# Optimization experiments

Measured on AMD Instinct MI355X. Metric: run time of the kernel, lower is better.

The kernel has to match this reference:

```python
import jax, jax.numpy as jnp
import numpy as np

B, T, V, D, E = 128, 50, 10000, 512, 2048


def setup_inputs() -> dict:
    key = jax.random.key(0)
    ks = jax.random.split(key, 14)
    s = 1.0 / np.sqrt(D)
    enc_out = jax.random.normal(ks[0], (B, E), jnp.float32)
    captions = jax.random.randint(ks[1], (B, T), 0, V)
    caplens = jax.random.randint(ks[2], (B, 1), 2, T + 1)
    caplens = caplens.at[0, 0].set(T)  # ensure max(caplens)-1 == T-1 (static shape)
    return {
        "enc_out": enc_out,
        "captions": captions,
        "caplens": caplens,
        "emb_W": jax.random.normal(ks[3], (V, D), jnp.float32),
        "W_ih": jax.random.uniform(ks[4], (4 * D, D), jnp.float32, -s, s),
        "W_hh": jax.random.uniform(ks[5], (4 * D, D), jnp.float32, -s, s),
        "b_ih": jax.random.uniform(ks[6], (4 * D,), jnp.float32, -s, s),
        "b_hh": jax.random.uniform(ks[7], (4 * D,), jnp.float32, -s, s),
        "fc_W": jax.random.uniform(ks[8], (V, D), jnp.float32, -s, s),
        "fc_b": jnp.zeros((V,), jnp.float32),
        "init_h_W": jax.random.uniform(ks[9], (D, E), jnp.float32, -s, s),
        "init_h_b": jnp.zeros((D,), jnp.float32),
        "init_c_W": jax.random.uniform(ks[10], (D, E), jnp.float32, -s, s),
        "init_c_b": jnp.zeros((D,), jnp.float32),
    }


def reference(enc_out, captions, caplens, emb_W, W_ih, W_hh, b_ih, b_hh,
              fc_W, fc_b, init_h_W, init_h_b, init_c_W, init_c_b):
    # Sort by caption length, descending (manual packing in the torch code).
    cl = caplens[:, 0]
    sort_idx = jnp.argsort(-cl)
    cl = cl[sort_idx]
    enc = enc_out[sort_idx]
    caps = captions[sort_idx]

    # init_states
    h0 = enc @ init_h_W.T + init_h_b  # [B, D]
    c0 = enc @ init_c_W.T + init_c_b

    emb = emb_W[caps]                  # [B, T, D] embedding gather
    dec_lens = cl - 1                  # decode lengths, max == T-1 by construction
    Tm = caps.shape[1] - 1             # static max timesteps

    # active-row mask per timestep: row b is active at step t iff t < dec_lens[b]
    masks = jnp.arange(Tm)[:, None] < dec_lens[None, :]   # [Tm, B]
    xs = jnp.moveaxis(emb[:, :Tm, :], 1, 0)               # [Tm, B, D]

    def step(carry, inp):
        h, c = carry
        x_t, m = inp                                      # [B,D], [B]
        gates = x_t @ W_ih.T + b_ih + h @ W_hh.T + b_hh   # [B, 4D]
        i, f, g, o = jnp.split(gates, 4, axis=-1)
        i = jax.nn.sigmoid(i)
        f = jax.nn.sigmoid(f)
        g = jnp.tanh(g)
        o = jax.nn.sigmoid(o)
        c_new = f * c + i * g
        h_new = o * jnp.tanh(c_new)
        mm = m[:, None]
        # inactive (shorter) rows keep their old state; torch never touches them
        h = jnp.where(mm, h_new, h)
        c = jnp.where(mm, c_new, c)
        # dropout in eval mode == identity; preds only written for active rows
        preds = jnp.where(mm, h_new @ fc_W.T + fc_b, 0.0)  # [B, V]
        return (h, c), preds

    (_, _), preds = jax.lax.scan(step, (h0, c0), (xs, masks))  # [Tm, B, V]
    predictions = jnp.moveaxis(preds, 0, 1)                    # [B, Tm, V]
    return predictions, caps, dec_lens, sort_idx
```

## Files before the change

### kernel.cpp

```cpp
#include <hip/hip_runtime.h>
#include <hip/hip_bf16.h>
#include <math.h>

typedef __attribute__((ext_vector_type(8))) short short8;
typedef __attribute__((ext_vector_type(4))) float f32x4;
typedef __attribute__((ext_vector_type(4))) unsigned short us4;
typedef unsigned short u16;
typedef unsigned long long u64;

#define TM 49
#define NV 10000
#define NLSTM 64
#define NFC 192
#define SMEM_BYTES 133184

__device__ __forceinline__ u16 f2bf(float f) {
    union { float f; unsigned u; } v; v.f = f;
    unsigned r = v.u + 0x7fffu + ((v.u >> 16) & 1u);
    return (u16)(r >> 16);
}
__device__ __forceinline__ float fsigm(float x) {
    return 1.0f / (1.0f + __expf(-x));
}
__device__ __forceinline__ float ftanh(float x) {
    float x2 = fminf(fmaxf(x + x, -30.0f), 30.0f);
    float e = __expf(x2);
    return (e - 1.0f) / (e + 1.0f);
}

__device__ __forceinline__ short8 ld_cp128(const u16* p) {
    short8 r;
    asm volatile("global_load_dwordx4 %0, %1, off sc0 sc1" : "=v"(r) : "v"(p));
    return r;
}
__device__ __forceinline__ void st_cp16(u16* p, unsigned v) {
    asm volatile("global_store_short %0, %1, off sc0 sc1" :: "v"(p), "v"(v) : "memory");
}
__device__ __forceinline__ void st_cp32f(float* p, float v) {
    asm volatile("global_store_dword %0, %1, off sc0 sc1" :: "v"(p), "v"(v) : "memory");
}
__device__ __forceinline__ void st_cp32u(unsigned* p, unsigned v) {
    asm volatile("global_store_dword %0, %1, off sc0 sc1" :: "v"(p), "v"(v) : "memory");
}
__device__ __forceinline__ unsigned ld_cp32_wait(const unsigned* p) {
    unsigned r;
    asm volatile("global_load_dword %0, %1, off sc0 sc1\n\ts_waitcnt vmcnt(0)"
                 : "=v"(r) : "v"(p) : "memory");
    return r;
}

__global__ __launch_bounds__(128) void k_sort(
    const int* __restrict__ caplens, const int* __restrict__ captions,
    const float* __restrict__ bih, const float* __restrict__ bhh,
    int* __restrict__ sidx, int* __restrict__ decl, int* __restrict__ capsS,
    float* __restrict__ bsum, float* __restrict__ out_tail,
    unsigned* __restrict__ flags, unsigned* __restrict__ xcnt,
    int* __restrict__ offs, int* __restrict__ rowmap, int* __restrict__ maskmap)
{
    __shared__ int s_cl[128];
    __shared__ int s_si[128];
    __shared__ int s_dl[128];
    __shared__ int s_n[49];
    __shared__ int s_off[50];
    __shared__ int s_moff[128];
    int tid = threadIdx.x;
    for (int k = tid; k < 2048; k += 128)
        __hip_atomic_store(&flags[k], 0u, __ATOMIC_RELAXED, __HIP_MEMORY_SCOPE_AGENT);
    for (int k = tid; k < 1568; k += 128)
        __hip_atomic_store(&xcnt[k], 0u, __ATOMIC_RELAXED, __HIP_MEMORY_SCOPE_AGENT);
    int my = caplens[tid];
    s_cl[tid] = my;
    __syncthreads();
    int r = 0;
    for (int j = 0; j < 128; j++) {
        int cj = s_cl[j];
        if (cj > my || (cj == my && j < tid)) r++;
    }
    s_si[r] = tid;
    __syncthreads();
    int src = s_si[tid];
    sidx[tid] = src;
    int dl = s_cl[src] - 1;
    decl[tid] = dl;
    s_dl[tid] = dl;
    out_tail[6400 + tid] = (float)dl;
    out_tail[6528 + tid] = (float)src;
    for (int t = 0; t < 50; t++) {
        int tok = captions[src * 50 + t];
        capsS[tid * 50 + t] = tok;
        out_tail[tid * 50 + t] = (float)tok;
    }
    for (int k = tid; k < 2048; k += 128) bsum[k] = bih[k] + bhh[k];
    __syncthreads();
    if (tid < 49) {
        int c = 0;
        for (int b = 0; b < 128; b++) c += (s_dl[b] > tid);
        s_n[tid] = c;
    }
    __syncthreads();
    if (tid == 0) {
        int a = 0;
        for (int t = 0; t < 49; t++) { s_off[t] = a; a += s_n[t]; }
        s_off[49] = a;
        int m = 0;
        for (int b = 0; b < 128; b++) { s_moff[b] = m; m += 49 - s_dl[b]; }
    }
    __syncthreads();
    if (tid < 50) offs[tid] = s_off[tid];
    for (int t = 0; t < dl; t++) rowmap[s_off[t] + tid] = t * 128 + tid;
    int mo = s_moff[tid];
    for (int t = dl; t < 49; t++) maskmap[mo + (t - dl)] = tid * 49 + t;
}

__global__ __launch_bounds__(256) void k_cvt(
    const float* __restrict__ Wih, const float* __restrict__ Whh,
    const float* __restrict__ fcW, const float* __restrict__ ihW,
    const float* __restrict__ icW,
    u16* __restrict__ WihB, u16* __restrict__ WhhB,
    u16* __restrict__ fcWB, u16* __restrict__ WhcB)
{
    int idx = blockIdx.x * 256 + threadIdx.x;
    const float* src; u16* dst; int o;
    if (idx < 262144)        { src = Wih; dst = WihB; o = idx; }
    else if (idx < 524288)   { src = Whh; dst = WhhB; o = idx - 262144; }
    else if (idx < 1804288)  { src = fcW; dst = fcWB; o = idx - 524288; }
    else if (idx < 2066432)  { src = ihW; dst = WhcB; o = idx - 1804288; }
    else                     { src = icW; dst = WhcB + 1048576; o = idx - 2066432; }
    f32x4 v = *(const f32x4*)&src[(size_t)o * 4];
    us4 b = { f2bf(v.x), f2bf(v.y), f2bf(v.z), f2bf(v.w) };
    *(us4*)&dst[(size_t)o * 4] = b;
}

__global__ __launch_bounds__(256) void k_gather(
    const float* __restrict__ enc, const float* __restrict__ embW,
    const int* __restrict__ sidx, const int* __restrict__ capsS,
    u16* __restrict__ encB, u16* __restrict__ Xemb)
{
    int idx = blockIdx.x * 256 + threadIdx.x;
    if (idx < 65536) {
        int b = idx >> 9, k4 = idx & 511;
        f32x4 v = *(const f32x4*)&enc[(size_t)sidx[b] * 2048 + k4 * 4];
        us4 o = { f2bf(v.x), f2bf(v.y), f2bf(v.z), f2bf(v.w) };
        *(us4*)&encB[(size_t)b * 2048 + k4 * 4] = o;
    } else {
        int j = idx - 65536;
        int row = j >> 7, k4 = j & 127;
        int t = row >> 7, b = row & 127;
        int tok = capsS[b * 50 + t];
        f32x4 v = *(const f32x4*)&embW[(size_t)tok * 512 + k4 * 4];
        us4 o = { f2bf(v.x), f2bf(v.y), f2bf(v.z), f2bf(v.w) };
        *(us4*)&Xemb[(size_t)row * 512 + k4 * 4] = o;
    }
}

__device__ __forceinline__ void tile_gemm_plain(
    const u16* __restrict__ A, int lda, const u16* __restrict__ B, int ldb,
    int K, int tid, u16 (*As)[40], u16 (*Bs)[40], f32x4 acc[4][4])
{
    const int w = tid >> 6, l = tid & 63;
    const int wr = (w >> 1) * 64, wc = (w & 1) * 64;
    const int lr = l & 15, lg = l >> 4;
    for (int k0 = 0; k0 < K; k0 += 32) {
        __syncthreads();
        #pragma unroll
        for (int i = 0; i < 2; i++) {
            int L = tid * 8 + i * 2048;
            int r = L >> 5, c = L & 31;
            *(short8*)&As[r][c] = *(const short8*)&A[(size_t)r * lda + k0 + c];
            *(short8*)&Bs[r][c] = *(const short8*)&B[(size_t)r * ldb + k0 + c];
        }
        __syncthreads();
        short8 af[4], bfr[4];
        #pragma unroll
        for (int m = 0; m < 4; m++) af[m] = *(const short8*)&As[wr + m * 16 + lr][lg * 8];
        #pragma unroll
        for (int n = 0; n < 4; n++) bfr[n] = *(const short8*)&Bs[wc + n * 16 + lr][lg * 8];
        #pragma unroll
        for (int m = 0; m < 4; m++)
            #pragma unroll
            for (int n = 0; n < 4; n++)
                acc[m][n] = __builtin_amdgcn_mfma_f32_16x16x32_bf16(af[m], bfr[n], acc[m][n], 0, 0, 0);
    }
}

__global__ __launch_bounds__(256, 1) void lstm_fc(
    const u16* __restrict__ Whh, float* __restrict__ X,
    u16* __restrict__ hb0, u16* __restrict__ hb1,
    u16* __restrict__ HnewC,
    const int* __restrict__ decl, unsigned* __restrict__ flags,
    unsigned* __restrict__ xcnt,
    const int* __restrict__ offs, const int* __restrict__ rowmap,
    const int* __restrict__ maskmap,
    const u16* __restrict__ fcWB, const float* __restrict__ fcb,
    const u16* __restrict__ encB, const u16* __restrict__ WhcB,
    const u16* __restrict__ WihB, const u16* __restrict__ Xemb,
    const float* __restrict__ bsum,
    const float* __restrict__ ihb, const float* __restrict__ icb,
    float* __restrict__ out)
{
    extern __shared__ char smem[];
    const int tid = threadIdx.x;
    const int wg = blockIdx.x;

    if (wg < NLSTM) {
        u16 (*As)[520] = (u16(*)[520])smem;
        u16 (*Bsi)[520] = (u16(*)[520])(smem + 33280);
        const int rb = wg >> 4, cb = wg & 15;
        const int w = tid >> 6, l = tid & 63;
        const int hi = w >> 1, lo = w & 1;
        const int lr = l & 15, lg = l >> 4;
        unsigned* myflag = &flags[(rb * 16 + cb) * 32];

        const int col = cb * 32 + lo * 16 + lr;
        int rowg[4];
        #pragma unroll
        for (int i = 0; i < 4; i++) rowg[i] = rb * 32 + hi * 16 + lg * 4 + i;

        f32x4 acch = {}, accc = {};
        for (int kq = 0; kq < 4; kq++) {
            __syncthreads();
            #pragma unroll
            for (int i = 0; i < 8; i++) {
                int L = tid * 8 + i * 2048;
                int r = L >> 9, cc = L & 511;
                *(short8*)&As[r][cc] =
                    *(const short8*)&encB[(size_t)(rb * 32 + r) * 2048 + kq * 512 + cc];
                *(short8*)&Bsi[r][cc] =
                    *(const short8*)&WhcB[(size_t)(cb * 32 + r) * 2048 + kq * 512 + cc];
            }
            __syncthreads();
            #pragma unroll
            for (int kk = 0; kk < 16; kk++) {
                short8 a = *(const short8*)&As[hi * 16 + lr][kk * 32 + lg * 8];
                short8 b = *(const short8*)&Bsi[lo * 16 + lr][kk * 32 + lg * 8];
                acch = __builtin_amdgcn_mfma_f32_16x16x32_bf16(a, b, acch, 0, 0, 0);
            }
            __syncthreads();
            #pragma unroll
            for (int i = 0; i < 8; i++) {
                int L = tid * 8 + i * 2048;
                int r = L >> 9, cc = L & 511;
                *(short8*)&Bsi[r][cc] =
                    *(const short8*)&WhcB[(size_t)(512 + cb * 32 + r) * 2048 + kq * 512 + cc];
            }
            __syncthreads();
            #pragma unroll
            for (int kk = 0; kk < 16; kk++) {
                short8 a = *(const short8*)&As[hi * 16 + lr][kk * 32 + lg * 8];
                short8 b = *(const short8*)&Bsi[lo * 16 + lr][kk * 32 + lg * 8];
                accc = __builtin_amdgcn_mfma_f32_16x16x32_bf16(a, b, accc, 0, 0, 0);
            }
        }

        int edec[4];
        f32x4 creg;
        us4 hreg;
        #pragma unroll
        for (int i = 0; i < 4; i++) {
            edec[i] = decl[rowg[i]];
            creg[i] = accc[i] + icb[col];
            hreg[i] = f2bf(acch[i] + ihb[col]);
            st_cp16(&hb0[(size_t)rowg[i] * 512 + col], (unsigned)hreg[i]);
        }
        asm volatile("s_waitcnt vmcnt(0)" ::: "memory");
        __syncthreads();
        if (tid == 0) st_cp32u(myflag, 1u);

        short8 bq[4][16];
        #pragma unroll
        for (int q = 0; q < 4; q++) {
            const u16* base = &Whh[(size_t)(q * 512 + cb * 32 + lo * 16 + lr) * 512 + lg * 8];
            #pragma unroll
            for (int kk = 0; kk < 16; kk++)
                bq[q][kk] = *(const short8*)&base[kk * 32];
        }
        #pragma unroll
        for (int q = 0; q < 4; q++)
            #pragma unroll
            for (int kk = 0; kk < 16; kk++)
                asm volatile("" : "+v"(bq[q][kk]));

        for (int t = 0; t < TM; t++) {
            const u16* hin = (t & 1) ? hb1 : hb0;
            u16* hout = (t & 1) ? hb0 : hb1;

            if (tid < 64) {
                unsigned tgt_h = (unsigned)(t + 1);
                while (true) {
                    bool ok = true;
                    if (tid < 16)
                        ok = (ld_cp32_wait(&flags[(rb * 16 + tid) * 32]) >= tgt_h);
                    else if (tid == 16)
                        ok = (ld_cp32_wait(&xcnt[t * 32]) >= 16u);
                    if (__all(ok)) break;
                }
            }
            __syncthreads();

            float xq[4][4];
            #pragma unroll
            for (int q = 0; q < 4; q++)
                #pragma unroll
                for (int i = 0; i < 4; i++)
                    xq[q][i] = X[(size_t)t * 262144 + (size_t)rowg[i] * 2048 + q * 512 + col];
            int offt = offs[t];

            short8 tmp[8];
            #pragma unroll
            for (int i = 0; i < 8; i++) {
                int L = i * 256 + tid;
                int r = L >> 6, cc = (L & 63) * 8;
                tmp[i] = ld_cp128(&hin[(size_t)(rb * 32 + r) * 512 + cc]);
            }
            asm volatile("s_waitcnt vmcnt(0)" ::: "memory");
            __builtin_amdgcn_sched_barrier(0);
            #pragma unroll
            for (int i = 0; i < 8; i++) {
                int L = i * 256 + tid;
                int r = L >> 6, cc = (L & 63) * 8;
                *(short8*)&As[r][cc] = tmp[i];
            }
            __syncthreads();

            f32x4 acc[4] = {};
            #pragma unroll
            for (int kk = 0; kk < 16; kk++) {
                short8 a = *(const short8*)&As[hi * 16 + lr][kk * 32 + lg * 8];
                acc[0] = __builtin_amdgcn_mfma_f32_16x16x32_bf16(a, bq[0][kk], acc[0], 0, 0, 0);
                acc[1] = __builtin_amdgcn_mfma_f32_16x16x32_bf16(a, bq[1][kk], acc[1], 0, 0, 0);
                acc[2] = __builtin_amdgcn_mfma_f32_16x16x32_bf16(a, bq[2][kk], acc[2], 0, 0, 0);
                acc[3] = __builtin_amdgcn_mfma_f32_16x16x32_bf16(a, bq[3][kk], acc[3], 0, 0, 0);
            }

            #pragma unroll
            for (int i = 0; i < 4; i++) {
                int act = (t < edec[i]);
                float iv = fsigm(acc[0][i] + xq[0][i]);
                float fv = fsigm(acc[1][i] + xq[1][i]);
                float gv = ftanh(acc[2][i] + xq[2][i]);
                float ov = fsigm(acc[3][i] + xq[3][i]);
                float cn = fv * creg[i] + iv * gv;
                float hn_f = ov * ftanh(cn);
                if (act) {
                    creg[i] = cn;
                    hreg[i] = f2bf(hn_f);
                }
                st_cp16(&hout[(size_t)rowg[i] * 512 + col], (unsigned)hreg[i]);
            }

            asm volatile("s_waitcnt vmcnt(0)" ::: "memory");
            __syncthreads();
            if (tid == 0) st_cp32u(myflag, (unsigned)(t + 2));
            #pragma unroll
            for (int i = 0; i < 4; i++)
                if (t < edec[i])
                    st_cp16(&HnewC[(size_t)(offt + rowg[i]) * 512 + col], (unsigned)hreg[i]);
        }

        asm volatile("s_waitcnt vmcnt(0)" ::: "memory");
        __syncthreads();
        if (tid == 0) st_cp32u(myflag, (unsigned)(TM + 2));
    } else {
        const int f = wg - NLSTM;
        const int w = tid >> 6, l = tid & 63;
        const int wr = (w >> 1) * 64, wc = (w & 1) * 64;
        const int lr = l & 15, lg = l >> 4;

        int nrC = offs[49];
        int nzero = 6272 - nrC;
        int nrt = (nrC + 127) >> 7;

        {
            u16 (*As)[40] = (u16(*)[40])smem;
            u16 (*Bs)[40] = (u16(*)[40])(smem + 10240);
            for (int j = f; j < 784; j += NFC) {
                int tt = j >> 4, cbx = j & 15;
                f32x4 acc[4][4] = {};
                tile_gemm_plain(Xemb + (size_t)tt * 128 * 512, 512,
                                WihB + (size_t)cbx * 128 * 512, 512,
                                512, tid, As, Bs, acc);
                #pragma unroll
                for (int m = 0; m < 4; m++)
                    #pragma unroll
                    for (int n = 0; n < 4; n++)
                        #pragma unroll
                        for (int i = 0; i < 4; i++) {
                            int row = wr + m * 16 + lg * 4 + i;
                            int colg = cbx * 128 + wc + n * 16 + lr;
                            st_cp32f(&X[(size_t)tt * 262144 + (size_t)row * 2048 + colg],
                                     acc[m][n][i] + bsum[colg]);
                        }
                asm volatile("s_waitcnt vmcnt(0)" ::: "memory");
                __syncthreads();
                if (tid == 0) atomicAdd(&xcnt[tt * 32], 1u);
            }
        }

        int c = f % 79;
        int sub = f / 79;
        int gsize = (c < 34) ? 3 : 2;

        u16 (*BT)[520] = (u16(*)[520])smem;
        unsigned* s_rdy = (unsigned*)(smem + 133120);
        __syncthreads();
        #pragma unroll
        for (int i = 0; i < 32; i++) {
            int L = i * 256 + tid;
            int r = L >> 6, cc = (L & 63) * 8;
            int gn = c * 128 + r;
            short8 b = {};
            if (gn < NV) b = *(const short8*)&fcWB[(size_t)gn * 512 + cc];
            *(short8*)&BT[r][cc] = b;
        }
        __syncthreads();

        int znext = f;
        f32x4 zv = {};

        for (int rt = sub; rt < nrt; rt += gsize) {
            int lastrow = min(rt * 128 + 127, nrC - 1);
            int tmax = rowmap[lastrow] >> 7;
            unsigned tgt = (unsigned)(tmax + 3);

            while (true) {
                bool ok = (tid < 64) ? (ld_cp32_wait(&flags[tid * 32]) >= tgt) : true;
                int allv = __all(ok);
                if (tid == 0) *s_rdy = (unsigned)allv;
                __syncthreads();
                bool rdy = (*s_rdy != 0);
                __syncthreads();
                if (rdy) break;
                if (znext < nzero) {
                    float* dst = out + (size_t)maskmap[znext] * 10000;
                    for (int i = tid; i < 2500; i += 256)
                        __builtin_nontemporal_store(zv, (f32x4*)&dst[i * 4]);
                    znext += NFC;
                } else {
                    __builtin_amdgcn_s_sleep(32);
                }
            }

            f32x4 acc[4][4] = {};
            #pragma unroll
            for (int ks = 0; ks < 16; ks++) {
                short8 af[4], bfr[4];
                #pragma unroll
                for (int m = 0; m < 4; m++) {
                    int gr = rt * 128 + wr + m * 16 + lr;
                    short8 a = {};
                    if (gr < nrC)
                        a = *(const short8*)&HnewC[(size_t)gr * 512 + ks * 32 + lg * 8];
                    af[m] = a;
                }
                #pragma unroll
                for (int n = 0; n < 4; n++)
                    bfr[n] = *(const short8*)&BT[wc + n * 16 + lr][ks * 32 + lg * 8];
                #pragma unroll
                for (int m = 0; m < 4; m++)
                    #pragma unroll
                    for (int n = 0; n < 4; n++)
                        acc[m][n] = __builtin_amdgcn_mfma_f32_16x16x32_bf16(af[m], bfr[n], acc[m][n], 0, 0, 0);
            }

            #pragma unroll
            for (int m = 0; m < 4; m++)
                #pragma unroll
                for (int n = 0; n < 4; n++)
                    #pragma unroll
                    for (int i = 0; i < 4; i++) {
                        int row = rt * 128 + wr + m * 16 + lg * 4 + i;
                        int colg = c * 128 + wc + n * 16 + lr;
                        if (row < nrC && colg < NV) {
                            int map = rowmap[row];
                            int b = map & 127, tt = map >> 7;
                            __builtin_nontemporal_store(
                                acc[m][n][i] + fcb[colg],
                                &out[(size_t)(b * 49 + tt) * 10000 + colg]);
                        }
                    }
        }

        while (znext < nzero) {
            float* dst = out + (size_t)maskmap[znext] * 10000;
            for (int i = tid; i < 2500; i += 256)
                __builtin_nontemporal_store(zv, (f32x4*)&dst[i * 4]);
            znext += NFC;
        }
    }
}

extern "C" void kernel_launch(void* const* d_in, const int* in_sizes, int n_in,
                              void* d_out, int out_size, void* d_ws, size_t ws_size,
                              hipStream_t stream) {
    const float* enc      = (const float*)d_in[0];
    const int*   captions = (const int*)d_in[1];
    const int*   caplens  = (const int*)d_in[2];
    const float* embW     = (const float*)d_in[3];
    const float* Wih      = (const float*)d_in[4];
    const float* Whh      = (const float*)d_in[5];
    const float* bih      = (const float*)d_in[6];
    const float* bhh      = (const float*)d_in[7];
    const float* fcW      = (const float*)d_in[8];
    const float* fcb      = (const float*)d_in[9];
    const float* ihW      = (const float*)d_in[10];
    const float* ihb      = (const float*)d_in[11];
    const float* icW      = (const float*)d_in[12];
    const float* icb      = (const float*)d_in[13];
    float* out = (float*)d_out;

    char* ws = (char*)d_ws;
    u16*   WihB = (u16*)(ws + 0);
    u16*   WhhB = (u16*)(ws + 2097152);
    u16*   fcWB = (u16*)(ws + 4194304);
    u16*   WhcB = (u16*)(ws + 14434304);
    u16*   encB = (u16*)(ws + 18628608);
    u16*   Xemb = (u16*)(ws + 19152896);
    float* X    = (float*)(ws + 25575424);
    u16*   HnewC= (u16*)(ws + 76955648);
    u16*   hb0  = (u16*)(ws + 83378176);
    u16*   hb1  = (u16*)(ws + 83509248);
    unsigned* flags = (unsigned*)(ws + 83640320);
    int*   sidx = (int*)(ws + 83902464);
    int*   decl = (int*)(ws + 83902976);
    int*   capsS= (int*)(ws + 83903488);
    float* bsum = (float*)(ws + 83929088);
    int*   offs   = (int*)(ws + 83938304);
    int*   rowmap = (int*)(ws + 83938560);
    int*   maskmap= (int*)(ws + 83963648);
    unsigned* xcnt = (unsigned*)(ws + 83988736);

    k_sort<<<1, 128, 0, stream>>>(caplens, captions, bih, bhh, sidx, decl, capsS, bsum,
                                  out + 62720000, flags, xcnt, offs, rowmap, maskmap);
    k_cvt<<<9096, 256, 0, stream>>>(Wih, Whh, fcW, ihW, icW, WihB, WhhB, fcWB, WhcB);
    k_gather<<<3392, 256, 0, stream>>>(enc, embW, sidx, capsS, encB, Xemb);
    lstm_fc<<<NLSTM + NFC, 256, SMEM_BYTES, stream>>>(
        WhhB, X, hb0, hb1, HnewC, decl, flags, xcnt, offs, rowmap, maskmap,
        fcWB, fcb, encB, WhcB, WihB, Xemb, bsum, ihb, icb, out);
}
```

Measured before the change: 332.1 us.

## Transpose MFMA operands so each lane owns one row and stores 4 columns

Swaps the A/B operands of the LSTM MFMAs so each lane's accumulator holds four consecutive columns of a single batch row. The per-step h writes, HnewC writes and X/bias loads then become one 64-bit store or 128-bit load instead of four scattered 16-bit or 32-bit accesses, and the active mask is a single scalar per lane. The per-workgroup flags are also packed contiguously instead of padded 128 bytes apart, which shrinks the polling footprint but may add cache-line contention between flag writers and pollers.

```diff
diff --git a/kernel.cpp b/kernel.cpp
--- a/kernel.cpp
+++ b/kernel.cpp
@@ -14,6 +14,8 @@
 #define NFC 192
 #define SMEM_BYTES 133184
 
+union U64c { us4 v; u64 u; };
+
 __device__ __forceinline__ u16 f2bf(float f) {
     union { float f; unsigned u; } v; v.f = f;
     unsigned r = v.u + 0x7fffu + ((v.u >> 16) & 1u);
@@ -33,8 +35,9 @@
     asm volatile("global_load_dwordx4 %0, %1, off sc0 sc1" : "=v"(r) : "v"(p));
     return r;
 }
-__device__ __forceinline__ void st_cp16(u16* p, unsigned v) {
-    asm volatile("global_store_short %0, %1, off sc0 sc1" :: "v"(p), "v"(v) : "memory");
+__device__ __forceinline__ void st_cp64(u16* p, us4 v) {
+    U64c u; u.v = v;
+    asm volatile("global_store_dwordx2 %0, %1, off sc0 sc1" :: "v"(p), "v"(u.u) : "memory");
 }
 __device__ __forceinline__ void st_cp32f(float* p, float v) {
     asm volatile("global_store_dword %0, %1, off sc0 sc1" :: "v"(p), "v"(v) : "memory");
@@ -64,8 +67,8 @@
     __shared__ int s_off[50];
     __shared__ int s_moff[128];
     int tid = threadIdx.x;
-    for (int k = tid; k < 2048; k += 128)
-        __hip_atomic_store(&flags[k], 0u, __ATOMIC_RELAXED, __HIP_MEMORY_SCOPE_AGENT);
+    if (tid < 64)
+        __hip_atomic_store(&flags[tid], 0u, __ATOMIC_RELAXED, __HIP_MEMORY_SCOPE_AGENT);
     for (int k = tid; k < 1568; k += 128)
         __hip_atomic_store(&xcnt[k], 0u, __ATOMIC_RELAXED, __HIP_MEMORY_SCOPE_AGENT);
     int my = caplens[tid];
@@ -209,12 +212,10 @@
         const int w = tid >> 6, l = tid & 63;
         const int hi = w >> 1, lo = w & 1;
         const int lr = l & 15, lg = l >> 4;
-        unsigned* myflag = &flags[(rb * 16 + cb) * 32];
-
-        const int col = cb * 32 + lo * 16 + lr;
-        int rowg[4];
-        #pragma unroll
-        for (int i = 0; i < 4; i++) rowg[i] = rb * 32 + hi * 16 + lg * 4 + i;
+        unsigned* myflag = &flags[wg];
+
+        const int r = rb * 32 + hi * 16 + lr;
+        const int col0 = cb * 32 + lo * 16 + lg * 4;
 
         f32x4 acch = {}, accc = {};
         for (int kq = 0; kq < 4; kq++) {
@@ -222,45 +223,48 @@
             #pragma unroll
             for (int i = 0; i < 8; i++) {
                 int L = tid * 8 + i * 2048;
-                int r = L >> 9, cc = L & 511;
-                *(short8*)&As[r][cc] =
-                    *(const short8*)&encB[(size_t)(rb * 32 + r) * 2048 + kq * 512 + cc];
-                *(short8*)&Bsi[r][cc] =
-                    *(const short8*)&WhcB[(size_t)(cb * 32 + r) * 2048 + kq * 512 + cc];
+                int rr = L >> 9, cc = L & 511;
+                *(short8*)&As[rr][cc] =
+                    *(const short8*)&encB[(size_t)(rb * 32 + rr) * 2048 + kq * 512 + cc];
+                *(short8*)&Bsi[rr][cc] =
+                    *(const short8*)&WhcB[(size_t)(cb * 32 + rr) * 2048 + kq * 512 + cc];
             }
             __syncthreads();
             #pragma unroll
             for (int kk = 0; kk < 16; kk++) {
                 short8 a = *(const short8*)&As[hi * 16 + lr][kk * 32 + lg * 8];
                 short8 b = *(const short8*)&Bsi[lo * 16 + lr][kk * 32 + lg * 8];
-                acch = __builtin_amdgcn_mfma_f32_16x16x32_bf16(a, b, acch, 0, 0, 0);
+                acch = __builtin_amdgcn_mfma_f32_16x16x32_bf16(b, a, acch, 0, 0, 0);
             }
             __syncthreads();
             #pragma unroll
             for (int i = 0; i < 8; i++) {
                 int L = tid * 8 + i * 2048;
-                int r = L >> 9, cc = L & 511;
-                *(short8*)&Bsi[r][cc] =
-                    *(const short8*)&WhcB[(size_t)(512 + cb * 32 + r) * 2048 + kq * 512 + cc];
+                int rr = L >> 9, cc = L & 511;
+                *(short8*)&Bsi[rr][cc] =
+                    *(const short8*)&WhcB[(size_t)(512 + cb * 32 + rr) * 2048 + kq * 512 + cc];
             }
             __syncthreads();
             #pragma unroll
             for (int kk = 0; kk < 16; kk++) {
                 short8 a = *(const short8*)&As[hi * 16 + lr][kk * 32 + lg * 8];
                 short8 b = *(const short8*)&Bsi[lo * 16 + lr][kk * 32 + lg * 8];
-                accc = __builtin_amdgcn_mfma_f32_16x16x32_bf16(a, b, accc, 0, 0, 0);
-            }
-        }
-
-        int edec[4];
+                accc = __builtin_amdgcn_mfma_f32_16x16x32_bf16(b, a, accc, 0, 0, 0);
+            }
+        }
+
+        const int edec = decl[r];
         f32x4 creg;
         us4 hreg;
-        #pragma unroll
-        for (int i = 0; i < 4; i++) {
-            edec[i] = decl[rowg[i]];
-            creg[i] = accc[i] + icb[col];
-            hreg[i] = f2bf(acch[i] + ihb[col]);
-            st_cp16(&hb0[(size_t)rowg[i] * 512 + col], (unsigned)hreg[i]);
+        {
+            f32x4 ihb4 = *(const f32x4*)&ihb[col0];
+            f32x4 icb4 = *(const f32x4*)&icb[col0];
+            #pragma unroll
+            for (int i = 0; i < 4; i++) {
+                creg[i] = accc[i] + icb4[i];
+                hreg[i] = f2bf(acch[i] + ihb4[i]);
+            }
+            st_cp64(&hb0[(size_t)r * 512 + col0], hreg);
         }
         asm volatile("s_waitcnt vmcnt(0)" ::: "memory");
         __syncthreads();
@@ -289,7 +293,7 @@
                 while (true) {
                     bool ok = true;
                     if (tid < 16)
-                        ok = (ld_cp32_wait(&flags[(rb * 16 + tid) * 32]) >= tgt_h);
+                        ok = (ld_cp32_wait(&flags[rb * 16 + tid]) >= tgt_h);
                     else if (tid == 16)
                         ok = (ld_cp32_wait(&xcnt[t * 32]) >= 16u);
                     if (__all(ok)) break;
@@ -297,28 +301,26 @@
             }
             __syncthreads();
 
-            float xq[4][4];
+            f32x4 xq[4];
             #pragma unroll
             for (int q = 0; q < 4; q++)
-                #pragma unroll
-                for (int i = 0; i < 4; i++)
-                    xq[q][i] = X[(size_t)t * 262144 + (size_t)rowg[i] * 2048 + q * 512 + col];
+                xq[q] = *(const f32x4*)&X[(size_t)t * 262144 + (size_t)r * 2048 + q * 512 + col0];
             int offt = offs[t];
 
             short8 tmp[8];
             #pragma unroll
             for (int i = 0; i < 8; i++) {
                 int L = i * 256 + tid;
-                int r = L >> 6, cc = (L & 63) * 8;
-                tmp[i] = ld_cp128(&hin[(size_t)(rb * 32 + r) * 512 + cc]);
+                int rr = L >> 6, cc = (L & 63) * 8;
+                tmp[i] = ld_cp128(&hin[(size_t)(rb * 32 + rr) * 512 + cc]);
             }
             asm volatile("s_waitcnt vmcnt(0)" ::: "memory");
             __builtin_amdgcn_sched_barrier(0);
             #pragma unroll
             for (int i = 0; i < 8; i++) {
                 int L = i * 256 + tid;
-                int r = L >> 6, cc = (L & 63) * 8;
-                *(short8*)&As[r][cc] = tmp[i];
+                int rr = L >> 6, cc = (L & 63) * 8;
+                *(short8*)&As[rr][cc] = tmp[i];
             }
             __syncthreads();
 
@@ -326,15 +328,15 @@
             #pragma unroll
             for (int kk = 0; kk < 16; kk++) {
                 short8 a = *(const short8*)&As[hi * 16 + lr][kk * 32 + lg * 8];
-                acc[0] = __builtin_amdgcn_mfma_f32_16x16x32_bf16(a, bq[0][kk], acc[0], 0, 0, 0);
-                acc[1] = __builtin_amdgcn_mfma_f32_16x16x32_bf16(a, bq[1][kk], acc[1], 0, 0, 0);
-                acc[2] = __builtin_amdgcn_mfma_f32_16x16x32_bf16(a, bq[2][kk], acc[2], 0, 0, 0);
-                acc[3] = __builtin_amdgcn_mfma_f32_16x16x32_bf16(a, bq[3][kk], acc[3], 0, 0, 0);
-            }
-
+                acc[0] = __builtin_amdgcn_mfma_f32_16x16x32_bf16(bq[0][kk], a, acc[0], 0, 0, 0);
+                acc[1] = __builtin_amdgcn_mfma_f32_16x16x32_bf16(bq[1][kk], a, acc[1], 0, 0, 0);
+                acc[2] = __builtin_amdgcn_mfma_f32_16x16x32_bf16(bq[2][kk], a, acc[2], 0, 0, 0);
+                acc[3] = __builtin_amdgcn_mfma_f32_16x16x32_bf16(bq[3][kk], a, acc[3], 0, 0, 0);
+            }
+
+            const int act = (t < edec);
             #pragma unroll
             for (int i = 0; i < 4; i++) {
-                int act = (t < edec[i]);
                 float iv = fsigm(acc[0][i] + xq[0][i]);
                 float fv = fsigm(acc[1][i] + xq[1][i]);
                 float gv = ftanh(acc[2][i] + xq[2][i]);
@@ -345,16 +347,14 @@
                     creg[i] = cn;
                     hreg[i] = f2bf(hn_f);
                 }
-                st_cp16(&hout[(size_t)rowg[i] * 512 + col], (unsigned)hreg[i]);
-            }
+            }
+            st_cp64(&hout[(size_t)r * 512 + col0], hreg);
 
             asm volatile("s_waitcnt vmcnt(0)" ::: "memory");
             __syncthreads();
             if (tid == 0) st_cp32u(myflag, (unsigned)(t + 2));
-            #pragma unroll
-            for (int i = 0; i < 4; i++)
-                if (t < edec[i])
-                    st_cp16(&HnewC[(size_t)(offt + rowg[i]) * 512 + col], (unsigned)hreg[i]);
+            if (act)
+                st_cp64(&HnewC[(size_t)(offt + r) * 512 + col0], hreg);
         }
 
         asm volatile("s_waitcnt vmcnt(0)" ::: "memory");
@@ -406,11 +406,11 @@
         #pragma unroll
         for (int i = 0; i < 32; i++) {
             int L = i * 256 + tid;
-            int r = L >> 6, cc = (L & 63) * 8;
-            int gn = c * 128 + r;
+            int rr = L >> 6, cc = (L & 63) * 8;
+            int gn = c * 128 + rr;
             short8 b = {};
             if (gn < NV) b = *(const short8*)&fcWB[(size_t)gn * 512 + cc];
-            *(short8*)&BT[r][cc] = b;
+            *(short8*)&BT[rr][cc] = b;
         }
         __syncthreads();
 
@@ -423,7 +423,7 @@
             unsigned tgt = (unsigned)(tmax + 3);
 
             while (true) {
-                bool ok = (tid < 64) ? (ld_cp32_wait(&flags[tid * 32]) >= tgt) : true;
+                bool ok = (tid < 64) ? (ld_cp32_wait(&flags[tid]) >= tgt) : true;
                 int allv = __all(ok);
                 if (tid == 0) *s_rdy = (unsigned)allv;
                 __syncthreads();
```

Measured after the change: 362.9 us. +9.3%, slower.
